# Optimization experiments

Hardware: AMD Instinct MI355X
Metric: run time of the kernel (lower is better)

Reference implementation:

```python
import jax, jax.numpy as jnp
import numpy as np

NUM_HEADS = 16

def setup_inputs() -> dict:
    key = jax.random.key(0)
    ks = jax.random.split(key, 5)
    b, n, d = 2, 2048, 1024
    s = 0.02
    return {
        "x": jax.random.normal(ks[0], (b, n, d), jnp.float32),
        "wq": jax.random.normal(ks[1], (d, d), jnp.float32) * s,
        "wk": jax.random.normal(ks[2], (d, d), jnp.float32) * s,
        "wv": jax.random.normal(ks[3], (d, d), jnp.float32) * s,
        "wo": jax.random.normal(ks[4], (d, d), jnp.float32) * s,
        "bo": jnp.zeros((d,), jnp.float32),
    }

def reference(x, wq, wk, wv, wo, bo):
    b, n, c = x.shape
    h = NUM_HEADS
    hd = c // h
    scale = hd ** -0.5
    # qkv projections (qkv_bias=False); torch Linear computes x @ W.T
    def split_heads(t):
        return t.reshape(b, n, h, hd).transpose(0, 2, 1, 3)  # b h n d
    q = split_heads(x @ wq.T)
    k = split_heads(x @ wk.T)
    v = split_heads(x @ wv.T)
    dots = jnp.einsum('bhid,bhjd->bhij', q, k) * scale
    attn = jax.nn.softmax(dots, axis=-1)  # attn_drop=0 -> identity
    out = jnp.einsum('bhij,bhjd->bhid', attn, v)
    out = out.transpose(0, 2, 1, 3).reshape(b, n, c)
    out = out @ wo.T + bo  # proj_drop=0 -> identity
    return out
```

## Files before the change

kernel.cpp:

```cpp
#include <hip/hip_runtime.h>
#include <hip/hip_bf16.h>

typedef float f32x4 __attribute__((ext_vector_type(4)));
typedef short short8 __attribute__((ext_vector_type(8)));
typedef short short4v __attribute__((ext_vector_type(4)));

#define MFMA(a, b, c) __builtin_amdgcn_mfma_f32_16x16x32_bf16((a), (b), (c), 0, 0, 0)

#if __has_builtin(__builtin_amdgcn_exp2f)
#define EXP2(x) __builtin_amdgcn_exp2f(x)
#else
#define EXP2(x) exp2f(x)
#endif

#define B_  2
#define N_  2048
#define C_  1024
#define H_  16
#define HD_ 64
#define M_  (B_ * N_)

#define QSCALE 0.18033688011112042f

typedef const __attribute__((address_space(1))) void* gp_t;
typedef __attribute__((address_space(3))) void* sp_t;
#define GLL16(g, s) __builtin_amdgcn_global_load_lds((gp_t)(const void*)(g), (sp_t)(void*)(s), 16, 0, 0)

__device__ __forceinline__ short f2bf(float f) {
    union { float fv; unsigned u; } v; v.fv = f;
    unsigned r = v.u + 0x7fffu + ((v.u >> 16) & 1u);
    return (short)(r >> 16);
}
__device__ __forceinline__ unsigned pack_rne(float a, float b) {
    return (unsigned)(unsigned short)f2bf(a) | ((unsigned)(unsigned short)f2bf(b) << 16);
}

__global__ __launch_bounds__(256) void convert_kernel(
    const float* __restrict__ x,  const float* __restrict__ wq,
    const float* __restrict__ wk, const float* __restrict__ wv,
    const float* __restrict__ wo, short* __restrict__ dst)
{
    size_t e = ((size_t)blockIdx.x * 256 + threadIdx.x) * 8;
    const float* src; size_t off;
    if (e < 4194304)      { src = x;  off = e; }
    else if (e < 5242880) { src = wq; off = e - 4194304; }
    else if (e < 6291456) { src = wk; off = e - 5242880; }
    else if (e < 7340032) { src = wv; off = e - 6291456; }
    else                  { src = wo; off = e - 7340032; }
    float4 a = *(const float4*)(src + off);
    float4 b = *(const float4*)(src + off + 4);
    short8 s;
    s[0] = f2bf(a.x); s[1] = f2bf(a.y); s[2] = f2bf(a.z); s[3] = f2bf(a.w);
    s[4] = f2bf(b.x); s[5] = f2bf(b.y); s[6] = f2bf(b.z); s[7] = f2bf(b.w);
    *(short8*)(dst + e) = s;
}

__global__ __launch_bounds__(256) void qkv_gemm(
    const short* __restrict__ xb, const short* __restrict__ Wb,
    short* __restrict__ Qb, short* __restrict__ Kb, short* __restrict__ Vt)
{
    const int m0 = blockIdx.x * 128;
    const int n0 = blockIdx.y * 128;
    __shared__ short As[128 * 64];
    __shared__ short Bs[128 * 64];
    const int tid  = threadIdx.x;
    const int wave = tid >> 6, lane = tid & 63;
    const int quad = lane >> 4, l16 = lane & 15;
    const int wr = (wave >> 1) * 64, wc = (wave & 1) * 64;
    const int sw = l16 & 7;

    const int rS = tid >> 3;
    const int cS = (tid & 7) ^ (rS & 7);
    const short* A_src = xb + (size_t)(m0 + rS) * C_ + cS * 8;
    const short* B_src = Wb + (size_t)(n0 + rS) * C_ + cS * 8;

    f32x4 acc[4][4] = {};

    for (int kk = 0; kk < C_; kk += 64) {
        __syncthreads();
        #pragma unroll
        for (int it = 0; it < 4; ++it) {
            GLL16(A_src + (size_t)(it * 32) * C_ + kk, &As[it * 2048 + tid * 8]);
            GLL16(B_src + (size_t)(it * 32) * C_ + kk, &Bs[it * 2048 + tid * 8]);
        }
        __syncthreads();
        short8 af[4][2], bf[4][2];
        #pragma unroll
        for (int mi = 0; mi < 4; ++mi) {
            int row = (wr + mi * 16 + l16) * 64;
            af[mi][0] = *(const short8*)&As[row + ((quad    ) ^ sw) * 8];
            af[mi][1] = *(const short8*)&As[row + ((quad + 4) ^ sw) * 8];
        }
        #pragma unroll
        for (int ni = 0; ni < 4; ++ni) {
            int row = (wc + ni * 16 + l16) * 64;
            bf[ni][0] = *(const short8*)&Bs[row + ((quad    ) ^ sw) * 8];
            bf[ni][1] = *(const short8*)&Bs[row + ((quad + 4) ^ sw) * 8];
        }
        #pragma unroll
        for (int k2 = 0; k2 < 2; ++k2)
        #pragma unroll
        for (int mi = 0; mi < 4; ++mi)
        #pragma unroll
        for (int ni = 0; ni < 4; ++ni)
            acc[mi][ni] = MFMA(af[mi][k2], bf[ni][k2], acc[mi][ni]);
    }

    const int which = n0 >> 10;
    const int nb = n0 & 1023;
    #pragma unroll
    for (int mi = 0; mi < 4; ++mi)
    #pragma unroll
    for (int ni = 0; ni < 4; ++ni)
    #pragma unroll
    for (int r = 0; r < 4; ++r) {
        int m  = m0 + wr + mi * 16 + quad * 4 + r;
        int cc = nb + wc + ni * 16 + l16;
        float av = acc[mi][ni][r];
        if (which == 0) av *= QSCALE;
        short bv = f2bf(av);
        int bb = m >> 11, ns = m & (N_ - 1);
        int h = cc >> 6, d = cc & 63;
        size_t bh = (size_t)(bb * H_ + h);
        if (which == 0)      Qb[(bh * N_ + ns) * HD_ + d] = bv;
        else if (which == 1) Kb[(bh * N_ + ns) * HD_ + d] = bv;
        else                 Vt[(bh * HD_ + d) * N_ + ns] = bv;
    }
}

__global__ __launch_bounds__(256, 4) void attn_kernel(
    const short* __restrict__ Qb, const short* __restrict__ Kb,
    const short* __restrict__ Vt, short* __restrict__ Ob)
{
    const int bid = blockIdx.y * 32 + blockIdx.x;
    const int swz = (bid & 7) * 128 + (bid >> 3);
    const int bh = swz >> 5;
    const int i0 = (swz & 31) * 64;
    const int b = bh >> 4, h = bh & (H_ - 1);
    __shared__ short Qs[64 * 64];
    __shared__ short Ks[2][64 * 64];
    __shared__ short Vs[2][64 * 64];
    const int tid  = threadIdx.x;
    const int wave = tid >> 6, lane = tid & 63;
    const int quad = lane >> 4, l16 = lane & 15;
    const int sw = l16 & 7;

    const short* Qg = Qb + ((size_t)bh * N_ + i0) * HD_;
    const short* Kg = Kb + (size_t)bh * N_ * HD_;
    const short* Vg = Vt + (size_t)bh * HD_ * N_;

    const int row0 = tid >> 3,  c0 = (tid & 7) ^ (row0 & 7);
    const int row1 = row0 + 32, c1 = (tid & 7) ^ (row1 & 7);
    const short* KgA0 = Kg + row0 * HD_ + c0 * 8;
    const short* KgA1 = Kg + row1 * HD_ + c1 * 8;
    const short* VgA0 = Vg + (size_t)row0 * N_ + c0 * 8;
    const short* VgA1 = Vg + (size_t)row1 * N_ + c1 * 8;

    #pragma unroll
    for (int it = 0; it < 2; ++it) {
        int s = it * 256 + tid;
        int row = s >> 3, c = (s & 7) ^ (row & 7);
        GLL16(Qg + row * HD_ + c * 8, &Qs[s * 8]);
    }
    GLL16(KgA0, &Ks[0][tid * 8]);
    GLL16(KgA1, &Ks[0][(tid + 256) * 8]);
    GLL16(VgA0, &Vs[0][tid * 8]);
    GLL16(VgA1, &Vs[0][(tid + 256) * 8]);
    __syncthreads();

    short8 qf[2];
    {
        int row = (wave * 16 + l16) * 64;
        qf[0] = *(const short8*)&Qs[row + ((quad ^ sw) * 8)];
        qf[1] = *(const short8*)&Qs[row + (((quad + 4) ^ sw) * 8)];
    }

    f32x4 o[4] = {};
    float lrow = 0.f;

    for (int jt = 0; jt < N_ / 64; ++jt) {
        const int cur = jt & 1;
        if (jt + 1 < N_ / 64) {
            int j1 = (jt + 1) * 64;
            GLL16(KgA0 + (size_t)j1 * HD_, &Ks[cur ^ 1][tid * 8]);
            GLL16(KgA1 + (size_t)j1 * HD_, &Ks[cur ^ 1][(tid + 256) * 8]);
            GLL16(VgA0 + j1, &Vs[cur ^ 1][tid * 8]);
            GLL16(VgA1 + j1, &Vs[cur ^ 1][(tid + 256) * 8]);
        }
        const short* Kc = Ks[cur];
        const short* Vc = Vs[cur];

        #pragma unroll
        for (int half = 0; half < 2; ++half) {
            unsigned pq[4];
            #pragma unroll
            for (int nio = 0; nio < 2; ++nio) {
                int ni = half * 2 + nio;
                int krow = (ni * 16 + l16) * 64;
                short8 kf0 = *(const short8*)&Kc[krow + ((quad ^ sw) * 8)];
                short8 kf1 = *(const short8*)&Kc[krow + (((quad + 4) ^ sw) * 8)];
                f32x4 st = {0.f, 0.f, 0.f, 0.f};
                __builtin_amdgcn_s_setprio(1);
                st = MFMA(kf0, qf[0], st);
                st = MFMA(kf1, qf[1], st);
                __builtin_amdgcn_s_setprio(0);
                union { float f; unsigned u; } e0, e1, e2, e3;
                e0.f = EXP2(st[0]); e1.f = EXP2(st[1]);
                e2.f = EXP2(st[2]); e3.f = EXP2(st[3]);
                lrow += (e0.f + e1.f) + (e2.f + e3.f);
                pq[nio * 2]     = (e0.u >> 16) | (e1.u & 0xffff0000u);
                pq[nio * 2 + 1] = (e2.u >> 16) | (e3.u & 0xffff0000u);
            }
            #pragma unroll
            for (int di = 0; di < 4; ++di) {
                int vrow = (di * 16 + l16) * 64;
                int ch1 = (half * 4 +     (quad >> 1)) ^ sw;
                int ch2 = (half * 4 + 2 + (quad >> 1)) ^ sw;
                union { struct { short4v lo, hi; } p; short8 v; } va;
                va.p.lo = *(const short4v*)&Vc[vrow + ch1 * 8 + (quad & 1) * 4];
                va.p.hi = *(const short4v*)&Vc[vrow + ch2 * 8 + (quad & 1) * 4];
                union { unsigned u[4]; short8 v; } pb;
                pb.u[0] = pq[0]; pb.u[1] = pq[1];
                pb.u[2] = pq[2]; pb.u[3] = pq[3];
                __builtin_amdgcn_s_setprio(1);
                o[di] = MFMA(va.v, pb.v, o[di]);
                __builtin_amdgcn_s_setprio(0);
            }
        }
        __syncthreads();
    }

    {
        float l = lrow;
        l += __shfl_xor(l, 16, 64);
        l += __shfl_xor(l, 32, 64);
        float inv = 1.f / l;
        int ig = i0 + wave * 16 + l16;
        size_t base = ((size_t)(b * N_ + ig)) * C_ + h * HD_;
        #pragma unroll
        for (int di = 0; di < 4; ++di) {
            unsigned p01 = pack_rne(o[di][0] * inv, o[di][1] * inv);
            unsigned p23 = pack_rne(o[di][2] * inv, o[di][3] * inv);
            *(unsigned*)&Ob[base + di * 16 + quad * 4]     = p01;
            *(unsigned*)&Ob[base + di * 16 + quad * 4 + 2] = p23;
        }
    }
}

__global__ __launch_bounds__(256) void proj_gemm(
    const short* __restrict__ Ob, const short* __restrict__ wob,
    const float* __restrict__ bo, float* __restrict__ out)
{
    const int m0 = blockIdx.x * 64;
    const int n0 = blockIdx.y * 128;
    __shared__ short As[64 * 32];
    __shared__ short Bs[128 * 32];
    const int tid  = threadIdx.x;
    const int wave = tid >> 6, lane = tid & 63;
    const int quad = lane >> 4, l16 = lane & 15;
    const int wr = (wave >> 1) * 32, wc = (wave & 1) * 64;

    f32x4 acc[2][4] = {};

    for (int kk = 0; kk < C_; kk += 32) {
        __syncthreads();
        {
            int f = tid * 8;
            int row = f >> 5, col = f & 31;
            GLL16(Ob + (size_t)(m0 + row) * C_ + kk + col, &As[f]);
        }
        #pragma unroll
        for (int it = 0; it < 2; ++it) {
            int f = (it * 256 + tid) * 8;
            int row = f >> 5, col = f & 31;
            GLL16(wob + (size_t)(n0 + row) * C_ + kk + col, &Bs[f]);
        }
        __syncthreads();
        short8 af[2], bf[4];
        #pragma unroll
        for (int mi = 0; mi < 2; ++mi) af[mi] = *(const short8*)&As[(wr + mi * 16 + l16) * 32 + quad * 8];
        #pragma unroll
        for (int ni = 0; ni < 4; ++ni) bf[ni] = *(const short8*)&Bs[(wc + ni * 16 + l16) * 32 + quad * 8];
        #pragma unroll
        for (int mi = 0; mi < 2; ++mi)
        #pragma unroll
        for (int ni = 0; ni < 4; ++ni)
            acc[mi][ni] = MFMA(af[mi], bf[ni], acc[mi][ni]);
    }

    #pragma unroll
    for (int mi = 0; mi < 2; ++mi)
    #pragma unroll
    for (int ni = 0; ni < 4; ++ni)
    #pragma unroll
    for (int r = 0; r < 4; ++r) {
        int m = m0 + wr + mi * 16 + quad * 4 + r;
        int c = n0 + wc + ni * 16 + l16;
        out[(size_t)m * C_ + c] = acc[mi][ni][r] + bo[c];
    }
}

extern "C" void kernel_launch(void* const* d_in, const int* in_sizes, int n_in,
                              void* d_out, int out_size, void* d_ws, size_t ws_size,
                              hipStream_t stream) {
    const float* x  = (const float*)d_in[0];
    const float* wq = (const float*)d_in[1];
    const float* wk = (const float*)d_in[2];
    const float* wv = (const float*)d_in[3];
    const float* wo = (const float*)d_in[4];
    const float* bo = (const float*)d_in[5];
    float* out = (float*)d_out;

    short* xb  = (short*)d_ws;
    short* Wb  = xb  + 4194304;
    short* wob = Wb  + 3145728;
    short* Qb  = wob + 1048576;
    short* Kb  = Qb  + 4194304;
    short* Vt  = Kb  + 4194304;
    short* Obuf= Vt  + 4194304;

    dim3 blk(256);
    convert_kernel<<<4096, blk, 0, stream>>>(x, wq, wk, wv, wo, xb);
    qkv_gemm<<<dim3(M_ / 128, 3072 / 128), blk, 0, stream>>>(xb, Wb, Qb, Kb, Vt);
    attn_kernel<<<dim3(N_ / 64, B_ * H_), blk, 0, stream>>>(Qb, Kb, Vt, Obuf);
    proj_gemm<<<dim3(M_ / 64, C_ / 128), blk, 0, stream>>>(Obuf, wob, bo, out);
}
```

Measured before the change: 195.7 us.

## Load Q directly to registers, raise attention occupancy, widen proj GEMM K-tile

The attention kernel now loads its Q fragments straight from global memory into registers, dropping the Qs shared buffer. It also raises the launch-bounds occupancy hint from 4 to 5 blocks and packs the bf16 probabilities with a single byte-permute. Separately, the output projection GEMM doubles its K-tile to 64 with XOR-swizzled shared memory, which halves the number of barriers and reduces LDS bank conflicts. The risks are register pressure from the higher occupancy target and uncoalesced direct Q loads.

```diff
diff --git a/kernel.cpp b/kernel.cpp
--- a/kernel.cpp
+++ b/kernel.cpp
@@ -128,7 +128,7 @@
     }
 }
 
-__global__ __launch_bounds__(256, 4) void attn_kernel(
+__global__ __launch_bounds__(256, 5) void attn_kernel(
     const short* __restrict__ Qb, const short* __restrict__ Kb,
     const short* __restrict__ Vt, short* __restrict__ Ob)
 {
@@ -137,7 +137,6 @@
     const int bh = swz >> 5;
     const int i0 = (swz & 31) * 64;
     const int b = bh >> 4, h = bh & (H_ - 1);
-    __shared__ short Qs[64 * 64];
     __shared__ short Ks[2][64 * 64];
     __shared__ short Vs[2][64 * 64];
     const int tid  = threadIdx.x;
@@ -156,24 +155,18 @@
     const short* VgA0 = Vg + (size_t)row0 * N_ + c0 * 8;
     const short* VgA1 = Vg + (size_t)row1 * N_ + c1 * 8;
 
-    #pragma unroll
-    for (int it = 0; it < 2; ++it) {
-        int s = it * 256 + tid;
-        int row = s >> 3, c = (s & 7) ^ (row & 7);
-        GLL16(Qg + row * HD_ + c * 8, &Qs[s * 8]);
-    }
+    short8 qf[2];
+    {
+        const short* qrow = Qg + (wave * 16 + l16) * HD_;
+        qf[0] = *(const short8*)(qrow + quad * 8);
+        qf[1] = *(const short8*)(qrow + quad * 8 + 32);
+    }
+
     GLL16(KgA0, &Ks[0][tid * 8]);
     GLL16(KgA1, &Ks[0][(tid + 256) * 8]);
     GLL16(VgA0, &Vs[0][tid * 8]);
     GLL16(VgA1, &Vs[0][(tid + 256) * 8]);
     __syncthreads();
-
-    short8 qf[2];
-    {
-        int row = (wave * 16 + l16) * 64;
-        qf[0] = *(const short8*)&Qs[row + ((quad ^ sw) * 8)];
-        qf[1] = *(const short8*)&Qs[row + (((quad + 4) ^ sw) * 8)];
-    }
 
     f32x4 o[4] = {};
     float lrow = 0.f;
@@ -208,8 +201,8 @@
                 e0.f = EXP2(st[0]); e1.f = EXP2(st[1]);
                 e2.f = EXP2(st[2]); e3.f = EXP2(st[3]);
                 lrow += (e0.f + e1.f) + (e2.f + e3.f);
-                pq[nio * 2]     = (e0.u >> 16) | (e1.u & 0xffff0000u);
-                pq[nio * 2 + 1] = (e2.u >> 16) | (e3.u & 0xffff0000u);
+                pq[nio * 2]     = __builtin_amdgcn_perm(e1.u, e0.u, 0x07060302u);
+                pq[nio * 2 + 1] = __builtin_amdgcn_perm(e3.u, e2.u, 0x07060302u);
             }
             #pragma unroll
             for (int di = 0; di < 4; ++di) {
@@ -253,39 +246,49 @@
 {
     const int m0 = blockIdx.x * 64;
     const int n0 = blockIdx.y * 128;
-    __shared__ short As[64 * 32];
-    __shared__ short Bs[128 * 32];
+    __shared__ short As[64 * 64];
+    __shared__ short Bs[128 * 64];
     const int tid  = threadIdx.x;
     const int wave = tid >> 6, lane = tid & 63;
     const int quad = lane >> 4, l16 = lane & 15;
     const int wr = (wave >> 1) * 32, wc = (wave & 1) * 64;
+    const int sw = l16 & 7;
+
+    const int rS = tid >> 3;
+    const int cS = (tid & 7) ^ (rS & 7);
+    const short* A_src = Ob  + (size_t)(m0 + rS) * C_ + cS * 8;
+    const short* B_src = wob + (size_t)(n0 + rS) * C_ + cS * 8;
 
     f32x4 acc[2][4] = {};
 
-    for (int kk = 0; kk < C_; kk += 32) {
-        __syncthreads();
-        {
-            int f = tid * 8;
-            int row = f >> 5, col = f & 31;
-            GLL16(Ob + (size_t)(m0 + row) * C_ + kk + col, &As[f]);
-        }
-        #pragma unroll
-        for (int it = 0; it < 2; ++it) {
-            int f = (it * 256 + tid) * 8;
-            int row = f >> 5, col = f & 31;
-            GLL16(wob + (size_t)(n0 + row) * C_ + kk + col, &Bs[f]);
-        }
-        __syncthreads();
-        short8 af[2], bf[4];
-        #pragma unroll
-        for (int mi = 0; mi < 2; ++mi) af[mi] = *(const short8*)&As[(wr + mi * 16 + l16) * 32 + quad * 8];
-        #pragma unroll
-        for (int ni = 0; ni < 4; ++ni) bf[ni] = *(const short8*)&Bs[(wc + ni * 16 + l16) * 32 + quad * 8];
+    for (int kk = 0; kk < C_; kk += 64) {
+        __syncthreads();
+        GLL16(A_src + kk, &As[tid * 8]);
+        GLL16(A_src + (size_t)32 * C_ + kk, &As[(tid + 256) * 8]);
+        #pragma unroll
+        for (int it = 0; it < 4; ++it)
+            GLL16(B_src + (size_t)(it * 32) * C_ + kk, &Bs[it * 2048 + tid * 8]);
+        __syncthreads();
+        short8 af[2][2], bf[4][2];
+        #pragma unroll
+        for (int mi = 0; mi < 2; ++mi) {
+            int row = (wr + mi * 16 + l16) * 64;
+            af[mi][0] = *(const short8*)&As[row + ((quad    ) ^ sw) * 8];
+            af[mi][1] = *(const short8*)&As[row + ((quad + 4) ^ sw) * 8];
+        }
+        #pragma unroll
+        for (int ni = 0; ni < 4; ++ni) {
+            int row = (wc + ni * 16 + l16) * 64;
+            bf[ni][0] = *(const short8*)&Bs[row + ((quad    ) ^ sw) * 8];
+            bf[ni][1] = *(const short8*)&Bs[row + ((quad + 4) ^ sw) * 8];
+        }
+        #pragma unroll
+        for (int k2 = 0; k2 < 2; ++k2)
         #pragma unroll
         for (int mi = 0; mi < 2; ++mi)
         #pragma unroll
         for (int ni = 0; ni < 4; ++ni)
-            acc[mi][ni] = MFMA(af[mi], bf[ni], acc[mi][ni]);
+            acc[mi][ni] = MFMA(af[mi][k2], bf[ni][k2], acc[mi][ni]);
     }
 
     #pragma unroll
```

New measurement: 191.6 us. -2.1%, faster.
